# Kernel tuning notes

Hardware: AMD Instinct MI355X
Metric: run time of the kernel (lower is better)

Reference implementation:

```python
import jax, jax.numpy as jnp
import numpy as np

N = 8192
F_IN = 512
F_OUT = 512
DENSITY = 0.01


def setup_inputs() -> dict:
    key = jax.random.key(0)
    k_x, k_adj, k_w, k_b = jax.random.split(key, 4)
    input_features = jax.random.normal(k_x, (N, F_IN), dtype=jnp.float32)
    adj = (jax.random.uniform(k_adj, (N, N)) < DENSITY).astype(jnp.float32)
    idx = jnp.arange(N)
    adj = adj.at[idx, idx].set(1.0)
    # nn.Linear(in, out) params; W stored as [in, out] so hidden = x @ W + b
    W = jax.random.normal(k_w, (F_IN, F_OUT), dtype=jnp.float32) / np.sqrt(F_IN)
    b = jax.random.normal(k_b, (F_OUT,), dtype=jnp.float32) * 0.01
    return {"input_features": input_features, "adj": adj, "W": W, "b": b}


def reference(input_features, adj, W, b):
    # adj.to_dense().bool().float(): binarize any nonzero entry
    A = (adj != 0).astype(input_features.dtype)  # [N, N]
    hidden = input_features @ W + b              # [N, F_out]
    deg = jnp.sum(A, axis=0)                     # column sums, [N]
    return (A @ hidden) / deg[:, None]           # [N, F_out]
```

## Files before the change

kernel.cpp:

```cpp
#include <hip/hip_runtime.h>
#include <stdint.h>

#define N_NODES 8192
#define FEAT 512
#define QCAP 1024

__device__ __forceinline__ unsigned short f2bf(float f) {
  unsigned int u = __float_as_uint(f);
  u += 0x7fffu + ((u >> 16) & 1u);
  return (unsigned short)(u >> 16);
}
__device__ __forceinline__ float bflo(unsigned int u) { return __uint_as_float(u << 16); }
__device__ __forceinline__ float bfhi(unsigned int u) { return __uint_as_float(u & 0xffff0000u); }

typedef __attribute__((ext_vector_type(8))) short short8;
typedef __attribute__((ext_vector_type(4))) float floatx4;

__global__ __launch_bounds__(256) void prep_kernel(const float* __restrict__ W,
                                                   unsigned short* __restrict__ Wt,
                                                   unsigned int* __restrict__ deg) {
  int gid = blockIdx.x * 256 + threadIdx.x;
  int k = gid >> 9, n = gid & 511;
  Wt[n * 512 + k] = f2bf(W[gid]);
  if (gid < N_NODES) deg[gid] = 0u;
}

__global__ __launch_bounds__(512) void gemm_kernel(const float* __restrict__ x,
                                                   const unsigned short* __restrict__ Wt,
                                                   const float* __restrict__ bias,
                                                   unsigned short* __restrict__ hidden) {
  __shared__ __align__(16) unsigned short Ab[64][40];
  __shared__ __align__(16) unsigned short Bb[256][40];
  int t = threadIdx.x;
  int m0 = blockIdx.x * 64;
  int n0 = blockIdx.y * 256;
  int lane = t & 63, wave = t >> 6;
  int quad = lane >> 4, l15 = lane & 15;
  int wm = wave & 1, wn = wave >> 1;

  floatx4 acc[2][4];
#pragma unroll
  for (int i = 0; i < 2; ++i)
#pragma unroll
    for (int j = 0; j < 4; ++j) acc[i][j] = (floatx4)0.0f;

  int arow = t >> 3, ac = (t & 7) * 4;
  int brow = t >> 1, bc = (t & 1) * 16;
  const float* xa = x + (size_t)(m0 + arow) * 512 + ac;
  const unsigned short* wb = Wt + (size_t)(n0 + brow) * 512 + bc;

  for (int kt = 0; kt < 16; ++kt) {
    int k0 = kt * 32;
    __syncthreads();
    float4 av = *(const float4*)(xa + k0);
    uint2 aw;
    aw.x = (unsigned int)f2bf(av.x) | ((unsigned int)f2bf(av.y) << 16);
    aw.y = (unsigned int)f2bf(av.z) | ((unsigned int)f2bf(av.w) << 16);
    *(uint2*)&Ab[arow][ac] = aw;
    uint4 bv0 = *(const uint4*)(wb + k0);
    uint4 bv1 = *(const uint4*)(wb + k0 + 8);
    *(uint4*)&Bb[brow][bc] = bv0;
    *(uint4*)&Bb[brow][bc + 8] = bv1;
    __syncthreads();

    short8 af[2];
    short8 bfr[4];
#pragma unroll
    for (int im = 0; im < 2; ++im)
      af[im] = *(const short8*)&Ab[wm * 32 + im * 16 + l15][quad * 8];
#pragma unroll
    for (int jn = 0; jn < 4; ++jn)
      bfr[jn] = *(const short8*)&Bb[wn * 64 + jn * 16 + l15][quad * 8];
#pragma unroll
    for (int im = 0; im < 2; ++im)
#pragma unroll
      for (int jn = 0; jn < 4; ++jn)
        acc[im][jn] = __builtin_amdgcn_mfma_f32_16x16x32_bf16(af[im], bfr[jn], acc[im][jn], 0, 0, 0);
  }

#pragma unroll
  for (int jn = 0; jn < 4; ++jn) {
    int col = n0 + wn * 64 + jn * 16 + l15;
    float bb = bias[col];
#pragma unroll
    for (int im = 0; im < 2; ++im) {
#pragma unroll
      for (int rg = 0; rg < 4; ++rg) {
        int row = m0 + wm * 32 + im * 16 + quad * 4 + rg;
        hidden[(size_t)row * 512 + col] = f2bf(acc[im][jn][rg] + bb);
      }
    }
  }
}

__global__ __launch_bounds__(256) void gather_kernel(const float* __restrict__ adj,
                                                     const unsigned short* __restrict__ hidden,
                                                     float* __restrict__ out,
                                                     unsigned int* __restrict__ deg) {
  __shared__ unsigned int degl[N_NODES];
  __shared__ unsigned short q[4][QCAP];
  int tid = threadIdx.x;
#pragma unroll
  for (int i = 0; i < 32; ++i) degl[i * 256 + tid] = 0u;
  __syncthreads();

  int lane = tid & 63, wave = tid >> 6;
  unsigned short* wq = q[wave];
  unsigned long long lanemask = (1ull << lane) - 1ull;
  int rbase = blockIdx.x * 8 + wave * 2;

  for (int rr = 0; rr < 2; ++rr) {
    int r = rbase + rr;
    const float4* __restrict__ arow = (const float4*)(adj + ((size_t)r << 13));
    float acc[8] = {0.f, 0.f, 0.f, 0.f, 0.f, 0.f, 0.f, 0.f};
    int qcnt = 0;

    auto drain = [&](int cnt) {
      int i = 0;
      for (; i + 8 <= cnt; i += 8) {
        int jj[8];
#pragma unroll
        for (int d = 0; d < 8; ++d) jj[d] = wq[i + d];
        uint2 h0[8], h1[8];
#pragma unroll
        for (int d = 0; d < 8; ++d) {
          const uint2* hp = (const uint2*)(hidden + ((size_t)jj[d] << 9));
          h0[d] = hp[lane];
          h1[d] = hp[64 + lane];
        }
#pragma unroll
        for (int d = 0; d < 8; ++d) {
          acc[0] += bflo(h0[d].x); acc[1] += bfhi(h0[d].x);
          acc[2] += bflo(h0[d].y); acc[3] += bfhi(h0[d].y);
          acc[4] += bflo(h1[d].x); acc[5] += bfhi(h1[d].x);
          acc[6] += bflo(h1[d].y); acc[7] += bfhi(h1[d].y);
        }
      }
      for (; i < cnt; ++i) {
        int j = wq[i];
        const uint2* hp = (const uint2*)(hidden + ((size_t)j << 9));
        uint2 h0 = hp[lane], h1 = hp[64 + lane];
        acc[0] += bflo(h0.x); acc[1] += bfhi(h0.x);
        acc[2] += bflo(h0.y); acc[3] += bfhi(h0.y);
        acc[4] += bflo(h1.x); acc[5] += bfhi(h1.x);
        acc[6] += bflo(h1.y); acc[7] += bfhi(h1.y);
      }
    };

    float4 cur = arow[lane];
    for (int ch = 0; ch < 32; ++ch) {
      float4 nxt = make_float4(0.f, 0.f, 0.f, 0.f);
      if (ch < 31) nxt = arow[(ch + 1) * 64 + lane];
      if (qcnt > QCAP - 256) { drain(qcnt); qcnt = 0; }
      int cbase = ch * 256 + 4 * lane;
#pragma unroll
      for (int e = 0; e < 4; ++e) {
        float val = (e == 0) ? cur.x : (e == 1) ? cur.y : (e == 2) ? cur.z : cur.w;
        bool nz = (val != 0.0f);
        unsigned long long m = __ballot(nz);
        if (nz) {
          atomicAdd(&degl[cbase + e], 1u);
          wq[qcnt + __popcll(m & lanemask)] = (unsigned short)(cbase + e);
        }
        qcnt += __popcll(m);
      }
      cur = nxt;
    }

    drain(qcnt);

    float4* orow = (float4*)(out + ((size_t)r << 9));
    orow[lane] = make_float4(acc[0], acc[1], acc[2], acc[3]);
    orow[64 + lane] = make_float4(acc[4], acc[5], acc[6], acc[7]);
  }

  __syncthreads();
#pragma unroll
  for (int i = 0; i < 32; ++i) {
    unsigned int c = degl[i * 256 + tid];
    if (c) atomicAdd(&deg[i * 256 + tid], c);
  }
}

__global__ __launch_bounds__(256) void norm_kernel(float* __restrict__ out,
                                                   const unsigned int* __restrict__ deg) {
  int lane = threadIdx.x & 63, wave = threadIdx.x >> 6;
  int r = blockIdx.x * 4 + wave;
  float s = 1.0f / (float)deg[r];
  float4* p = (float4*)(out + ((size_t)r << 9));
  float4 v0 = p[lane], v1 = p[64 + lane];
  v0.x *= s; v0.y *= s; v0.z *= s; v0.w *= s;
  v1.x *= s; v1.y *= s; v1.z *= s; v1.w *= s;
  p[lane] = v0;
  p[64 + lane] = v1;
}

extern "C" void kernel_launch(void* const* d_in, const int* in_sizes, int n_in,
                              void* d_out, int out_size, void* d_ws, size_t ws_size,
                              hipStream_t stream) {
  const float* x   = (const float*)d_in[0];
  const float* adj = (const float*)d_in[1];
  const float* W   = (const float*)d_in[2];
  const float* b   = (const float*)d_in[3];
  float* out = (float*)d_out;

  char* ws = (char*)d_ws;
  unsigned short* hidden = (unsigned short*)ws;
  unsigned short* Wt     = (unsigned short*)(ws + (size_t)N_NODES * FEAT * 2);
  unsigned int*   deg    = (unsigned int*)(ws + (size_t)N_NODES * FEAT * 2 + (size_t)FEAT * FEAT * 2);

  prep_kernel<<<1024, 256, 0, stream>>>(W, Wt, deg);
  gemm_kernel<<<dim3(128, 2), 512, 0, stream>>>(x, Wt, b, hidden);
  gather_kernel<<<1024, 256, 0, stream>>>(adj, hidden, out, deg);
  norm_kernel<<<2048, 256, 0, stream>>>(out, deg);
}
```

Before: 448.0 us.

## Interleave adjacency scan with hidden gathers via ring queue, one row per wave

The gather kernel now gives each wave one row with 512-thread blocks instead of two rows per wave, and prefetches two adjacency chunks ahead. Neighbor indices go into a circular queue that is drained in groups of eight while scanning continues, replacing the old scan-then-drain-in-bulk pattern. Each lane loads one contiguous 16-byte slice of the hidden row instead of two 8-byte pieces. The intent is to overlap the streaming adjacency reads with the random hidden-row gathers and to raise wave-level parallelism. The ring queue relies on the backlog never exceeding its 512 entries; the eager drain appears to keep it at most around 263.

```diff
diff --git a/kernel.cpp b/kernel.cpp
--- a/kernel.cpp
+++ b/kernel.cpp
@@ -3,7 +3,7 @@
 
 #define N_NODES 8192
 #define FEAT 512
-#define QCAP 1024
+#define QCAP 512
 
 __device__ __forceinline__ unsigned short f2bf(float f) {
   unsigned int u = __float_as_uint(f);
@@ -93,92 +93,80 @@
   }
 }
 
-__global__ __launch_bounds__(256) void gather_kernel(const float* __restrict__ adj,
+__global__ __launch_bounds__(512) void gather_kernel(const float* __restrict__ adj,
                                                      const unsigned short* __restrict__ hidden,
                                                      float* __restrict__ out,
                                                      unsigned int* __restrict__ deg) {
   __shared__ unsigned int degl[N_NODES];
-  __shared__ unsigned short q[4][QCAP];
+  __shared__ unsigned short q[8][QCAP];
   int tid = threadIdx.x;
 #pragma unroll
-  for (int i = 0; i < 32; ++i) degl[i * 256 + tid] = 0u;
+  for (int i = 0; i < 16; ++i) degl[i * 512 + tid] = 0u;
   __syncthreads();
 
   int lane = tid & 63, wave = tid >> 6;
   unsigned short* wq = q[wave];
   unsigned long long lanemask = (1ull << lane) - 1ull;
-  int rbase = blockIdx.x * 8 + wave * 2;
-
-  for (int rr = 0; rr < 2; ++rr) {
-    int r = rbase + rr;
-    const float4* __restrict__ arow = (const float4*)(adj + ((size_t)r << 13));
-    float acc[8] = {0.f, 0.f, 0.f, 0.f, 0.f, 0.f, 0.f, 0.f};
-    int qcnt = 0;
-
-    auto drain = [&](int cnt) {
-      int i = 0;
-      for (; i + 8 <= cnt; i += 8) {
-        int jj[8];
-#pragma unroll
-        for (int d = 0; d < 8; ++d) jj[d] = wq[i + d];
-        uint2 h0[8], h1[8];
-#pragma unroll
-        for (int d = 0; d < 8; ++d) {
-          const uint2* hp = (const uint2*)(hidden + ((size_t)jj[d] << 9));
-          h0[d] = hp[lane];
-          h1[d] = hp[64 + lane];
-        }
-#pragma unroll
-        for (int d = 0; d < 8; ++d) {
-          acc[0] += bflo(h0[d].x); acc[1] += bfhi(h0[d].x);
-          acc[2] += bflo(h0[d].y); acc[3] += bfhi(h0[d].y);
-          acc[4] += bflo(h1[d].x); acc[5] += bfhi(h1[d].x);
-          acc[6] += bflo(h1[d].y); acc[7] += bfhi(h1[d].y);
-        }
+  int r = blockIdx.x * 8 + wave;
+
+  const float4* __restrict__ arow = (const float4*)(adj + ((size_t)r << 13));
+  float acc[8] = {0.f, 0.f, 0.f, 0.f, 0.f, 0.f, 0.f, 0.f};
+  int qcnt = 0, qhead = 0;
+
+  float4 c0 = arow[lane];
+  float4 c1 = arow[64 + lane];
+  for (int ch = 0; ch < 32; ++ch) {
+    float4 nx = make_float4(0.f, 0.f, 0.f, 0.f);
+    if (ch < 30) nx = arow[(ch + 2) * 64 + lane];
+    int cbase = ch * 256 + 4 * lane;
+#pragma unroll
+    for (int e = 0; e < 4; ++e) {
+      float val = (e == 0) ? c0.x : (e == 1) ? c0.y : (e == 2) ? c0.z : c0.w;
+      bool nz = (val != 0.0f);
+      unsigned long long m = __ballot(nz);
+      if (nz) {
+        atomicAdd(&degl[cbase + e], 1u);
+        wq[(qcnt + __popcll(m & lanemask)) & (QCAP - 1)] = (unsigned short)(cbase + e);
       }
-      for (; i < cnt; ++i) {
-        int j = wq[i];
-        const uint2* hp = (const uint2*)(hidden + ((size_t)j << 9));
-        uint2 h0 = hp[lane], h1 = hp[64 + lane];
-        acc[0] += bflo(h0.x); acc[1] += bfhi(h0.x);
-        acc[2] += bflo(h0.y); acc[3] += bfhi(h0.y);
-        acc[4] += bflo(h1.x); acc[5] += bfhi(h1.x);
-        acc[6] += bflo(h1.y); acc[7] += bfhi(h1.y);
+      qcnt += __popcll(m);
+    }
+    c0 = c1; c1 = nx;
+    while (qcnt - qhead >= 8) {
+      int jj[8];
+#pragma unroll
+      for (int d = 0; d < 8; ++d) jj[d] = wq[(qhead + d) & (QCAP - 1)];
+      uint4 h[8];
+#pragma unroll
+      for (int d = 0; d < 8; ++d)
+        h[d] = ((const uint4*)(hidden + ((size_t)jj[d] << 9)))[lane];
+#pragma unroll
+      for (int d = 0; d < 8; ++d) {
+        acc[0] += bflo(h[d].x); acc[1] += bfhi(h[d].x);
+        acc[2] += bflo(h[d].y); acc[3] += bfhi(h[d].y);
+        acc[4] += bflo(h[d].z); acc[5] += bfhi(h[d].z);
+        acc[6] += bflo(h[d].w); acc[7] += bfhi(h[d].w);
       }
-    };
-
-    float4 cur = arow[lane];
-    for (int ch = 0; ch < 32; ++ch) {
-      float4 nxt = make_float4(0.f, 0.f, 0.f, 0.f);
-      if (ch < 31) nxt = arow[(ch + 1) * 64 + lane];
-      if (qcnt > QCAP - 256) { drain(qcnt); qcnt = 0; }
-      int cbase = ch * 256 + 4 * lane;
-#pragma unroll
-      for (int e = 0; e < 4; ++e) {
-        float val = (e == 0) ? cur.x : (e == 1) ? cur.y : (e == 2) ? cur.z : cur.w;
-        bool nz = (val != 0.0f);
-        unsigned long long m = __ballot(nz);
-        if (nz) {
-          atomicAdd(&degl[cbase + e], 1u);
-          wq[qcnt + __popcll(m & lanemask)] = (unsigned short)(cbase + e);
-        }
-        qcnt += __popcll(m);
-      }
-      cur = nxt;
+      qhead += 8;
     }
-
-    drain(qcnt);
-
-    float4* orow = (float4*)(out + ((size_t)r << 9));
-    orow[lane] = make_float4(acc[0], acc[1], acc[2], acc[3]);
-    orow[64 + lane] = make_float4(acc[4], acc[5], acc[6], acc[7]);
-  }
+  }
+  for (; qhead < qcnt; ++qhead) {
+    int j = wq[qhead & (QCAP - 1)];
+    uint4 h = ((const uint4*)(hidden + ((size_t)j << 9)))[lane];
+    acc[0] += bflo(h.x); acc[1] += bfhi(h.x);
+    acc[2] += bflo(h.y); acc[3] += bfhi(h.y);
+    acc[4] += bflo(h.z); acc[5] += bfhi(h.z);
+    acc[6] += bflo(h.w); acc[7] += bfhi(h.w);
+  }
+
+  float4* orow = (float4*)(out + ((size_t)r << 9));
+  orow[2 * lane]     = make_float4(acc[0], acc[1], acc[2], acc[3]);
+  orow[2 * lane + 1] = make_float4(acc[4], acc[5], acc[6], acc[7]);
 
   __syncthreads();
 #pragma unroll
-  for (int i = 0; i < 32; ++i) {
-    unsigned int c = degl[i * 256 + tid];
-    if (c) atomicAdd(&deg[i * 256 + tid], c);
+  for (int i = 0; i < 16; ++i) {
+    unsigned int c = degl[i * 512 + tid];
+    if (c) atomicAdd(&deg[i * 512 + tid], c);
   }
 }
 
@@ -211,6 +199,6 @@
 
   prep_kernel<<<1024, 256, 0, stream>>>(W, Wt, deg);
   gemm_kernel<<<dim3(128, 2), 512, 0, stream>>>(x, Wt, b, hidden);
-  gather_kernel<<<1024, 256, 0, stream>>>(adj, hidden, out, deg);
+  gather_kernel<<<1024, 512, 0, stream>>>(adj, hidden, out, deg);
   norm_kernel<<<2048, 256, 0, stream>>>(out, deg);
 }
```

Result: faster. 427.2 us (-4.6%).
